# Kernel optimization log

Measured on AMD Instinct MI355X. Metric: run time of the kernel, lower is better.

## Reference

```python
import jax, jax.numpy as jnp
import numpy as np

NUM_HEADS = 16
HEAD_DIM = 64  # hidden_size 1024 / 16 heads


def setup_inputs() -> dict:
    key = jax.random.key(0)
    ks = jax.random.split(key, 4)
    B, S, H = 2, 2048, 1024
    scale = 0.02
    return {
        "hidden_states": jax.random.normal(ks[0], (B, S, H), jnp.float32),
        "attention_mask": jnp.zeros((B, 1, 1, S), jnp.float32),  # additive mask
        "Wq": jax.random.normal(ks[1], (H, H), jnp.float32) * scale,
        "bq": jnp.zeros((H,), jnp.float32),
        "Wk": jax.random.normal(ks[2], (H, H), jnp.float32) * scale,
        "bk": jnp.zeros((H,), jnp.float32),
        "Wv": jax.random.normal(ks[3], (H, H), jnp.float32) * scale,
        "bv": jnp.zeros((H,), jnp.float32),
    }


def _split_heads(x):
    B, S, H = x.shape
    return x.reshape(B, S, NUM_HEADS, HEAD_DIM).transpose(0, 2, 1, 3)  # [B,h,S,dh]


def reference(hidden_states, attention_mask, Wq, bq, Wk, bk, Wv, bv):
    q = _split_heads(hidden_states @ Wq + bq)
    k = _split_heads(hidden_states @ Wk + bk)
    v = _split_heads(hidden_states @ Wv + bv)
    # scaled dot-product scores [B,h,S,S]
    scores = jnp.einsum("bhqd,bhkd->bhqk", q, k) / np.sqrt(HEAD_DIM).astype(np.float32)
    scores = scores + attention_mask  # additive mask, broadcast [B,1,1,S]
    probs = jax.nn.softmax(scores, axis=-1)  # dropout prob = 0.0
    ctx = jnp.einsum("bhqk,bhkd->bhqd", probs, v)
    B, h, S, dh = ctx.shape
    return ctx.transpose(0, 2, 1, 3).reshape(B, S, h * dh)  # [B,S,hidden]
```

## Files before the change

### kernel.cpp

```cpp
#include <hip/hip_runtime.h>
#include <hip/hip_bf16.h>


typedef __bf16 bf16x8 __attribute__((ext_vector_type(8)));
typedef __bf16 bf16x4 __attribute__((ext_vector_type(4)));
typedef float f32x4 __attribute__((ext_vector_type(4)));
typedef float f32x16 __attribute__((ext_vector_type(16)));
typedef int i32x4 __attribute__((ext_vector_type(4)));

static constexpr int H = 1024;
static constexpr int S = 2048;
static constexpr int NH = 16;
static constexpr int DH = 64;
static constexpr float L2E = 1.4426950408889634f;

#if __has_builtin(__builtin_amdgcn_exp2f)
#define EXP2F(x) __builtin_amdgcn_exp2f(x)
#else
#define EXP2F(x) __builtin_exp2f(x)
#endif

__device__ inline void gll16(const void* g, void* l) {
  __builtin_amdgcn_global_load_lds(
      (const __attribute__((address_space(1))) void*)g,
      (__attribute__((address_space(3))) void*)l, 16, 0, 0);
}

__device__ inline int pack2bf(float lo, float hi) {
  unsigned short a = __builtin_bit_cast(unsigned short, (__bf16)lo);
  unsigned short b = __builtin_bit_cast(unsigned short, (__bf16)hi);
  return (int)(((unsigned)b << 16) | (unsigned)a);
}

__device__ inline void plswap(int& a, int& b) {
  asm volatile("v_permlane32_swap_b32 %0, %1" : "+v"(a), "+v"(b));
}

__global__ __launch_bounds__(256) void convert_kernel(
    const float* __restrict__ X, const float* __restrict__ W0,
    const float* __restrict__ W1, const float* __restrict__ W2,
    __bf16* __restrict__ Xb, __bf16* __restrict__ Wt) {
  __shared__ float T[64][65];
  const int bid = blockIdx.x, tid = threadIdx.x;
  if (bid < 2048) {
    size_t i = ((size_t)bid * 256 + tid) * 8;
    float4 f0 = *(const float4*)(X + i);
    float4 f1 = *(const float4*)(X + i + 4);
    bf16x8 o;
    o[0] = (__bf16)f0.x; o[1] = (__bf16)f0.y; o[2] = (__bf16)f0.z; o[3] = (__bf16)f0.w;
    o[4] = (__bf16)f1.x; o[5] = (__bf16)f1.y; o[6] = (__bf16)f1.z; o[7] = (__bf16)f1.w;
    *(bf16x8*)(Xb + i) = o;
    return;
  }
  const int wid = bid - 2048;
  const int z = wid >> 8, t = wid & 255;
  const int k0 = (t >> 4) * 64, n0 = (t & 15) * 64;
  const float* W = z == 0 ? W0 : (z == 1 ? W1 : W2);
  __bf16* Wo = Wt + (size_t)z * H * H;
#pragma unroll
  for (int it = 0; it < 4; ++it) {
    int r = it * 16 + (tid >> 4), c = (tid & 15) * 4;
    *(float4*)&T[r][c] = *(const float4*)&W[(size_t)(k0 + r) * H + n0 + c];
  }
  __syncthreads();
#pragma unroll
  for (int it = 0; it < 4; ++it) {
    int n = it * 16 + (tid >> 4), c0 = (tid & 15) * 4;
    bf16x4 o;
#pragma unroll
    for (int j = 0; j < 4; ++j) o[j] = (__bf16)T[c0 + j][n];
    *(bf16x4*)&Wo[(size_t)(n0 + n) * H + k0 + c0] = o;
  }
}

__global__ __launch_bounds__(256, 3) void qkv_gemm_kernel(
    const __bf16* __restrict__ Xb, const __bf16* __restrict__ Wt,
    const float* __restrict__ bq, const float* __restrict__ bk,
    const float* __restrict__ bv,
    __bf16* __restrict__ Qt, __bf16* __restrict__ K, __bf16* __restrict__ Vt)
{
  __shared__ __bf16 As[128 * 64];
  __shared__ __bf16 Bs[128 * 64];

  const int tid = threadIdx.x, lane = tid & 63, w = tid >> 6;
  const int quad = lane >> 4, l16 = lane & 15;
  const int wsel = blockIdx.x >> 3;
  const int n0 = (blockIdx.x & 7) * 128;
  const int m0 = blockIdx.y * 128;
  const int wr = w & 1, wc = w >> 1;

  const __bf16* Wsel = Wt + (size_t)wsel * H * H;
  const float* bias = wsel == 0 ? bq : (wsel == 1 ? bk : bv);

  const __bf16* aptr[4];
  const __bf16* bptr[4];
#pragma unroll
  for (int i = 0; i < 4; ++i) {
    int s = w * 256 + i * 64 + lane;
    int row = s >> 3, col = s & 7, sc = col ^ (row & 7);
    aptr[i] = Xb + (size_t)(m0 + row) * H + sc * 8;
    bptr[i] = Wsel + (size_t)(n0 + row) * H + sc * 8;
  }

  f32x4 acc[4][4] = {};

  for (int k0 = 0; k0 < H; k0 += 64) {
    __syncthreads();
#pragma unroll
    for (int i = 0; i < 4; ++i) {
      gll16(aptr[i] + k0, &As[(w * 256 + i * 64) * 8]);
      gll16(bptr[i] + k0, &Bs[(w * 256 + i * 64) * 8]);
    }
    __syncthreads();
#pragma unroll
    for (int kc = 0; kc < 2; ++kc) {
      bf16x8 af[4], bfr[4];
#pragma unroll
      for (int t = 0; t < 4; ++t) {
        int ra = wr * 64 + t * 16 + l16;
        af[t] = *(const bf16x8*)&As[ra * 64 + (((kc * 4 + quad) ^ (ra & 7)) * 8)];
        int rb = wc * 64 + t * 16 + l16;
        bfr[t] = *(const bf16x8*)&Bs[rb * 64 + (((kc * 4 + quad) ^ (rb & 7)) * 8)];
      }
#pragma unroll
      for (int t = 0; t < 4; ++t)
#pragma unroll
        for (int u = 0; u < 4; ++u)
          acc[t][u] = __builtin_amdgcn_mfma_f32_16x16x32_bf16(af[t], bfr[u], acc[t][u], 0, 0, 0);
    }
  }

  const float qscale = 0.125f * L2E;
#pragma unroll
  for (int u = 0; u < 4; ++u) {
    int n = n0 + wc * 64 + u * 16 + l16;
    int head = n >> 6, d = n & 63;
    float bias_v = bias[n];
#pragma unroll
    for (int t = 0; t < 4; ++t) {
      int srow = m0 + wr * 64 + t * 16 + quad * 4;
      int b = srow >> 11, si = srow & (S - 1);
      int bh = b * NH + head;
      if (wsel == 1) {
        __bf16* dst = K + ((size_t)bh * S + si) * DH + d;
#pragma unroll
        for (int r = 0; r < 4; ++r)
          dst[(size_t)r * DH] = (__bf16)(acc[t][u][r] + bias_v);
      } else {
        float scl = wsel == 0 ? qscale : 1.0f;
        __bf16* outp = wsel == 0 ? Qt : Vt;
        bf16x4 o;
#pragma unroll
        for (int r = 0; r < 4; ++r) o[r] = (__bf16)((acc[t][u][r] + bias_v) * scl);
        *(bf16x4*)&outp[((size_t)bh * DH + d) * S + si] = o;
      }
    }
  }
}

__global__ __launch_bounds__(512, 4) void attn_kernel(
    const __bf16* __restrict__ Qt, const __bf16* __restrict__ K,
    const __bf16* __restrict__ Vt, const float* __restrict__ mask,
    float* __restrict__ out)
{
  __shared__ __bf16 SM[20480];
  __bf16* Ksb = SM;
  __bf16* Vsb = SM + 8192;
  float*  Ms  = (float*)(SM + 16384);

  const int tid = threadIdx.x, lane = tid & 63, w = tid >> 6;
  const int l31 = lane & 31, hi = lane >> 5;
  const int wl = w & 3, wh = w >> 2;

  const int lin = blockIdx.y * 16 + blockIdx.x;
  const int v = (lin & 7) * 64 + (lin >> 3);
  const int bh = v >> 4, b = bh >> 4, h = bh & 15;
  const int q0 = (v & 15) * 128;

  const __bf16* Qb = Qt + (size_t)bh * DH * S;
  const __bf16* Kb = K + (size_t)bh * S * DH;
  const __bf16* Vb = Vt + (size_t)bh * DH * S;
  const float* mb = mask + (size_t)b * S;

  {
    int idx = tid * 4;
    float4 mv = *(const float4*)&mb[idx];
    float4 sv = {mv.x * L2E, mv.y * L2E, mv.z * L2E, mv.w * L2E};
    *(float4*)&Ms[idx] = sv;
  }

  const int q = q0 + wl * 32 + l31;
  bf16x8 qf[4];
#pragma unroll
  for (int kc = 0; kc < 4; ++kc)
#pragma unroll
    for (int j = 0; j < 8; ++j)
      qf[kc][j] = Qb[(size_t)(kc * 16 + hi * 8 + j) * S + q];

  const int kvbase = wh * 1024;
  const __bf16* kptr[2];
  const __bf16* vptr[2];
#pragma unroll
  for (int i = 0; i < 2; ++i) {
    int s = wl * 128 + i * 64 + lane;
    int row = s >> 3, col = s & 7, sc = col ^ (row & 7);
    kptr[i] = Kb + (size_t)(kvbase + row) * DH + sc * 8;
    vptr[i] = Vb + (size_t)row * S + kvbase + sc * 8;
  }

  f32x16 o0 = {}, o1 = {};
  float dl = 0.0f;

  for (int st = 0; st < 16; ++st) {
    __syncthreads();
#pragma unroll
    for (int i = 0; i < 2; ++i) {
      gll16(kptr[i] + (size_t)st * 64 * DH,
            &Ksb[wh * 4096 + (wl * 128 + i * 64 + lane) * 8]);
      gll16(vptr[i] + st * 64,
            &Vsb[wh * 4096 + (wl * 128 + i * 64 + lane) * 8]);
    }
    __syncthreads();
    const __bf16* Kc = &Ksb[wh * 4096];
    const __bf16* Vc = &Vsb[wh * 4096];
    const int kvabs = kvbase + st * 64;

#pragma unroll
    for (int kvsub = 0; kvsub < 2; ++kvsub) {
      const int rk = kvsub * 32 + l31;
      f32x16 cc;
#pragma unroll
      for (int g = 0; g < 4; ++g) {
        float4 m4 = *(const float4*)&Ms[kvabs + kvsub * 32 + g * 8 + hi * 4];
        cc[4 * g + 0] = m4.x; cc[4 * g + 1] = m4.y;
        cc[4 * g + 2] = m4.z; cc[4 * g + 3] = m4.w;
      }
      __builtin_amdgcn_s_setprio(1);
#pragma unroll
      for (int kc = 0; kc < 4; ++kc) {
        bf16x8 af = *(const bf16x8*)&Kc[rk * 64 + (((kc * 2 + hi) ^ (l31 & 7)) * 8)];
        cc = __builtin_amdgcn_mfma_f32_32x32x16_bf16(af, qf[kc], cc, 0, 0, 0);
      }
      __builtin_amdgcn_s_setprio(0);

      float p[16];
#pragma unroll
      for (int r = 0; r < 16; ++r) { p[r] = EXP2F(cc[r]); dl += p[r]; }
      int a0 = pack2bf(p[0],  p[1]),  b0 = pack2bf(p[2],  p[3]);
      int a1 = pack2bf(p[4],  p[5]),  b1 = pack2bf(p[6],  p[7]);
      int a2 = pack2bf(p[8],  p[9]),  b2 = pack2bf(p[10], p[11]);
      int a3 = pack2bf(p[12], p[13]), b3 = pack2bf(p[14], p[15]);
      plswap(a0, a1); plswap(b0, b1);
      plswap(a2, a3); plswap(b2, b3);
      i32x4 pi0 = {a0, b0, a1, b1};
      i32x4 pi1 = {a2, b2, a3, b3};
      bf16x8 pf0 = __builtin_bit_cast(bf16x8, pi0);
      bf16x8 pf1 = __builtin_bit_cast(bf16x8, pi1);

      __builtin_amdgcn_s_setprio(1);
#pragma unroll
      for (int pp = 0; pp < 2; ++pp) {
        const int pc = kvsub * 2 + pp;
        const bf16x8 pf = pp ? pf1 : pf0;
        bf16x8 vf0 = *(const bf16x8*)&Vc[l31 * 64 + (((pc * 2 + hi) ^ (l31 & 7)) * 8)];
        o0 = __builtin_amdgcn_mfma_f32_32x32x16_bf16(vf0, pf, o0, 0, 0, 0);
        bf16x8 vf1 = *(const bf16x8*)&Vc[(32 + l31) * 64 + (((pc * 2 + hi) ^ (l31 & 7)) * 8)];
        o1 = __builtin_amdgcn_mfma_f32_32x32x16_bf16(vf1, pf, o1, 0, 0, 0);
      }
      __builtin_amdgcn_s_setprio(0);
    }
  }

  float lsum = dl + __shfl_xor(dl, 32);

  __syncthreads();
  float* Os = (float*)SM;
  float* Ls = Ms;
  if (wh == 1) {
#pragma unroll
    for (int g = 0; g < 4; ++g) {
      int s0 = (2 * g + hi) ^ (l31 & 7);
      float4 t0 = {o0[4 * g + 0], o0[4 * g + 1], o0[4 * g + 2], o0[4 * g + 3]};
      *(float4*)&Os[(wl * 32 + l31) * 64 + s0 * 4] = t0;
      int s1 = (8 + 2 * g + hi) ^ (l31 & 7);
      float4 t1 = {o1[4 * g + 0], o1[4 * g + 1], o1[4 * g + 2], o1[4 * g + 3]};
      *(float4*)&Os[(wl * 32 + l31) * 64 + s1 * 4] = t1;
    }
    if (hi == 0) Ls[wl * 32 + l31] = lsum;
  }
  __syncthreads();
  if (wh == 0) {
    float ltot = lsum + Ls[wl * 32 + l31];
    float invl = 1.0f / ltot;
#pragma unroll
    for (int g = 0; g < 4; ++g) {
      int d0 = g * 8 + hi * 4;
      int s0 = (2 * g + hi) ^ (l31 & 7);
      float4 u0 = *(const float4*)&Os[(wl * 32 + l31) * 64 + s0 * 4];
      float4 r0 = {(o0[4 * g + 0] + u0.x) * invl, (o0[4 * g + 1] + u0.y) * invl,
                   (o0[4 * g + 2] + u0.z) * invl, (o0[4 * g + 3] + u0.w) * invl};
      *(float4*)&out[((size_t)b * S + q) * H + h * DH + d0] = r0;
      int s1 = (8 + 2 * g + hi) ^ (l31 & 7);
      float4 u1 = *(const float4*)&Os[(wl * 32 + l31) * 64 + s1 * 4];
      float4 r1 = {(o1[4 * g + 0] + u1.x) * invl, (o1[4 * g + 1] + u1.y) * invl,
                   (o1[4 * g + 2] + u1.z) * invl, (o1[4 * g + 3] + u1.w) * invl};
      *(float4*)&out[((size_t)b * S + q) * H + h * DH + 32 + d0] = r1;
    }
  }
}

extern "C" void kernel_launch(void* const* d_in, const int* in_sizes, int n_in,
                              void* d_out, int out_size, void* d_ws, size_t ws_size,
                              hipStream_t stream) {
  const float* X    = (const float*)d_in[0];
  const float* mask = (const float*)d_in[1];
  const float* Wq   = (const float*)d_in[2];
  const float* bq   = (const float*)d_in[3];
  const float* Wk   = (const float*)d_in[4];
  const float* bk   = (const float*)d_in[5];
  const float* Wv   = (const float*)d_in[6];
  const float* bv   = (const float*)d_in[7];
  float* out = (float*)d_out;

  const size_t per = (size_t)2 * NH * S * DH;
  __bf16* Qws  = (__bf16*)d_ws;
  __bf16* Kws  = Qws + per;
  __bf16* Vtws = Kws + per;

  __bf16* Xb = (__bf16*)d_out;
  __bf16* Wt = Xb + per;

  convert_kernel<<<2816, 256, 0, stream>>>(X, Wq, Wk, Wv, Xb, Wt);
  qkv_gemm_kernel<<<dim3(24, 32), 256, 0, stream>>>(Xb, Wt, bq, bk, bv,
                                                    Qws, Kws, Vtws);
  attn_kernel<<<dim3(16, 32), 512, 0, stream>>>(Qws, Kws, Vtws, mask, out);
}
```

Baseline: 160.8 us.

## Split attention KV range across four wave groups with 1024-thread blocks

The attention kernel now launches 1024 threads per block, so four wave groups each process a quarter of the key/value sequence instead of two groups each handling half. Shared memory grows to hold K/V tiles for all four groups, and the partial outputs and row sums are combined through shared memory in a two-step tree reduction. This halves the serial KV loop per wave to add latency hiding and parallelism per query tile. In exchange it adds reduction passes and barriers, raises LDS use, and the launch bound of 1024 threads with 4 blocks may squeeze registers per thread.

```diff
diff --git a/kernel.cpp b/kernel.cpp
--- a/kernel.cpp
+++ b/kernel.cpp
@@ -158,15 +158,15 @@
   }
 }
 
-__global__ __launch_bounds__(512, 4) void attn_kernel(
+__global__ __launch_bounds__(1024, 4) void attn_kernel(
     const __bf16* __restrict__ Qt, const __bf16* __restrict__ K,
     const __bf16* __restrict__ Vt, const float* __restrict__ mask,
     float* __restrict__ out)
 {
-  __shared__ __bf16 SM[20480];
+  __shared__ __bf16 SM[36864];
   __bf16* Ksb = SM;
-  __bf16* Vsb = SM + 8192;
-  float*  Ms  = (float*)(SM + 16384);
+  __bf16* Vsb = SM + 16384;
+  float*  Ms  = (float*)(SM + 32768);
 
   const int tid = threadIdx.x, lane = tid & 63, w = tid >> 6;
   const int l31 = lane & 31, hi = lane >> 5;
@@ -182,7 +182,7 @@
   const __bf16* Vb = Vt + (size_t)bh * DH * S;
   const float* mb = mask + (size_t)b * S;
 
-  {
+  if (tid < 512) {
     int idx = tid * 4;
     float4 mv = *(const float4*)&mb[idx];
     float4 sv = {mv.x * L2E, mv.y * L2E, mv.z * L2E, mv.w * L2E};
@@ -197,7 +197,7 @@
     for (int j = 0; j < 8; ++j)
       qf[kc][j] = Qb[(size_t)(kc * 16 + hi * 8 + j) * S + q];
 
-  const int kvbase = wh * 1024;
+  const int kvbase = wh * 512;
   const __bf16* kptr[2];
   const __bf16* vptr[2];
 #pragma unroll
@@ -211,7 +211,7 @@
   f32x16 o0 = {}, o1 = {};
   float dl = 0.0f;
 
-  for (int st = 0; st < 16; ++st) {
+  for (int st = 0; st < 8; ++st) {
     __syncthreads();
 #pragma unroll
     for (int i = 0; i < 2; ++i) {
@@ -274,39 +274,63 @@
   float lsum = dl + __shfl_xor(dl, 32);
 
   __syncthreads();
-  float* Os = (float*)SM;
-  float* Ls = Ms;
-  if (wh == 1) {
-#pragma unroll
-    for (int g = 0; g < 4; ++g) {
-      int s0 = (2 * g + hi) ^ (l31 & 7);
-      float4 t0 = {o0[4 * g + 0], o0[4 * g + 1], o0[4 * g + 2], o0[4 * g + 3]};
-      *(float4*)&Os[(wl * 32 + l31) * 64 + s0 * 4] = t0;
-      int s1 = (8 + 2 * g + hi) ^ (l31 & 7);
-      float4 t1 = {o1[4 * g + 0], o1[4 * g + 1], o1[4 * g + 2], o1[4 * g + 3]};
-      *(float4*)&Os[(wl * 32 + l31) * 64 + s1 * 4] = t1;
-    }
-    if (hi == 0) Ls[wl * 32 + l31] = lsum;
-  }
+  float* Os0 = (float*)SM;
+  float* Os1 = (float*)(SM + 16384);
+  float* Ls  = (float*)(SM + 32768);
+  const int qi = wl * 32 + l31;
+
+#define WRITE_O(Os)                                                         \
+  {                                                                         \
+    _Pragma("unroll") for (int g = 0; g < 4; ++g) {                         \
+      int s0 = (2 * g + hi) ^ (l31 & 7);                                    \
+      float4 t0 = {o0[4 * g + 0], o0[4 * g + 1], o0[4 * g + 2],             \
+                   o0[4 * g + 3]};                                          \
+      *(float4*)&(Os)[qi * 64 + s0 * 4] = t0;                               \
+      int s1 = (8 + 2 * g + hi) ^ (l31 & 7);                                \
+      float4 t1 = {o1[4 * g + 0], o1[4 * g + 1], o1[4 * g + 2],             \
+                   o1[4 * g + 3]};                                          \
+      *(float4*)&(Os)[qi * 64 + s1 * 4] = t1;                               \
+    }                                                                       \
+  }
+#define ADD_O(Os)                                                           \
+  {                                                                         \
+    _Pragma("unroll") for (int g = 0; g < 4; ++g) {                         \
+      int s0 = (2 * g + hi) ^ (l31 & 7);                                    \
+      float4 u0 = *(const float4*)&(Os)[qi * 64 + s0 * 4];                  \
+      o0[4 * g + 0] += u0.x; o0[4 * g + 1] += u0.y;                         \
+      o0[4 * g + 2] += u0.z; o0[4 * g + 3] += u0.w;                         \
+      int s1 = (8 + 2 * g + hi) ^ (l31 & 7);                                \
+      float4 u1 = *(const float4*)&(Os)[qi * 64 + s1 * 4];                  \
+      o1[4 * g + 0] += u1.x; o1[4 * g + 1] += u1.y;                         \
+      o1[4 * g + 2] += u1.z; o1[4 * g + 3] += u1.w;                         \
+    }                                                                       \
+  }
+
+  if (wh == 2) { WRITE_O(Os0); if (hi == 0) Ls[128 + qi] = lsum; }
+  if (wh == 3) { WRITE_O(Os1); if (hi == 0) Ls[256 + qi] = lsum; }
+  __syncthreads();
+  if (wh == 0) { ADD_O(Os0); lsum += Ls[128 + qi]; }
+  if (wh == 1) { ADD_O(Os1); lsum += Ls[256 + qi]; }
+  __syncthreads();
+  if (wh == 1) { WRITE_O(Os0); if (hi == 0) Ls[qi] = lsum; }
   __syncthreads();
   if (wh == 0) {
-    float ltot = lsum + Ls[wl * 32 + l31];
-    float invl = 1.0f / ltot;
+    ADD_O(Os0);
+    lsum += Ls[qi];
+    float invl = 1.0f / lsum;
 #pragma unroll
     for (int g = 0; g < 4; ++g) {
       int d0 = g * 8 + hi * 4;
-      int s0 = (2 * g + hi) ^ (l31 & 7);
-      float4 u0 = *(const float4*)&Os[(wl * 32 + l31) * 64 + s0 * 4];
-      float4 r0 = {(o0[4 * g + 0] + u0.x) * invl, (o0[4 * g + 1] + u0.y) * invl,
-                   (o0[4 * g + 2] + u0.z) * invl, (o0[4 * g + 3] + u0.w) * invl};
+      float4 r0 = {o0[4 * g + 0] * invl, o0[4 * g + 1] * invl,
+                   o0[4 * g + 2] * invl, o0[4 * g + 3] * invl};
       *(float4*)&out[((size_t)b * S + q) * H + h * DH + d0] = r0;
-      int s1 = (8 + 2 * g + hi) ^ (l31 & 7);
-      float4 u1 = *(const float4*)&Os[(wl * 32 + l31) * 64 + s1 * 4];
-      float4 r1 = {(o1[4 * g + 0] + u1.x) * invl, (o1[4 * g + 1] + u1.y) * invl,
-                   (o1[4 * g + 2] + u1.z) * invl, (o1[4 * g + 3] + u1.w) * invl};
+      float4 r1 = {o1[4 * g + 0] * invl, o1[4 * g + 1] * invl,
+                   o1[4 * g + 2] * invl, o1[4 * g + 3] * invl};
       *(float4*)&out[((size_t)b * S + q) * H + h * DH + 32 + d0] = r1;
     }
   }
+#undef WRITE_O
+#undef ADD_O
 }
 
 extern "C" void kernel_launch(void* const* d_in, const int* in_sizes, int n_in,
@@ -333,5 +357,5 @@
   convert_kernel<<<2816, 256, 0, stream>>>(X, Wq, Wk, Wv, Xb, Wt);
   qkv_gemm_kernel<<<dim3(24, 32), 256, 0, stream>>>(Xb, Wt, bq, bk, bv,
                                                     Qws, Kws, Vtws);
-  attn_kernel<<<dim3(16, 32), 512, 0, stream>>>(Qws, Kws, Vtws, mask, out);
-}
+  attn_kernel<<<dim3(16, 32), 1024, 0, stream>>>(Qws, Kws, Vtws, mask, out);
+}
```

Result: slower. 167.8 us (+4.4%).
